# Kernel tuning notes

Hardware: AMD Instinct MI355X
Metric: run time of the kernel (lower is better)

The kernel has to match this reference:

```python
import jax, jax.numpy as jnp
import numpy as np

N = 100000   # nodes
E = 1600000  # edges
D = 64       # in_dim == hidden
H = 64       # hidden
L = 5        # GIN layers
G = 128      # graphs in batch
OUT = 10     # out_dim
BN_EPS = 1e-5


def setup_inputs() -> dict:
    key = jax.random.key(0)
    ks = jax.random.split(key, 16)
    x = jax.random.normal(ks[0], (N, D), dtype=jnp.float32)
    ei = jax.random.randint(ks[1], (2, E), 0, N, dtype=jnp.int64)
    b = jnp.sort(jax.random.randint(ks[2], (N,), 0, G, dtype=jnp.int64))
    s = 0.1
    return {
        "x": x,
        "ei": ei,
        "b": b,
        "conv_W1": jax.random.normal(ks[3], (L, D, H), dtype=jnp.float32) * s,
        "conv_b1": jnp.zeros((L, H), dtype=jnp.float32),
        "conv_W2": jax.random.normal(ks[4], (L, H, H), dtype=jnp.float32) * s,
        "conv_b2": jnp.zeros((L, H), dtype=jnp.float32),
        "bn_gamma": jnp.ones((L, H), dtype=jnp.float32),
        "bn_beta": jnp.zeros((L, H), dtype=jnp.float32),
        "head_W1": jax.random.normal(ks[5], (H, H), dtype=jnp.float32) * s,
        "head_b1": jnp.zeros((H,), dtype=jnp.float32),
        "head_W2": jax.random.normal(ks[6], (H, OUT), dtype=jnp.float32) * s,
        "head_b2": jnp.zeros((OUT,), dtype=jnp.float32),
    }


def reference(x, ei, b, conv_W1, conv_b1, conv_W2, conv_b2,
              bn_gamma, bn_beta, head_W1, head_b1, head_W2, head_b2):
    src, dst = ei[0], ei[1]
    for l in range(L):
        # GINConv (eps=0): h = x + sum_{j in N(i)} x_j  via gather + scatter-add
        agg = jax.ops.segment_sum(x[src], dst, num_segments=N)  # [N, d]
        h = x + agg
        # nn MLP: Linear -> ReLU -> Linear
        h = jax.nn.relu(h @ conv_W1[l] + conv_b1[l]) @ conv_W2[l] + conv_b2[l]
        # BatchNorm over node dim (batch statistics), then ReLU (dropout: eval)
        mean = jnp.mean(h, axis=0)
        var = jnp.var(h, axis=0)
        h = bn_gamma[l] * (h - mean) * jax.lax.rsqrt(var + BN_EPS) + bn_beta[l]
        x = jax.nn.relu(h)
    # global mean pool per graph
    sums = jax.ops.segment_sum(x, b, num_segments=G)                 # [G, H]
    cnts = jax.ops.segment_sum(jnp.ones((N,), x.dtype), b, num_segments=G)
    pooled = sums / jnp.maximum(cnts, 1.0)[:, None]
    # head: Linear -> ReLU -> (Dropout eval) -> Linear
    return jax.nn.relu(pooled @ head_W1 + head_b1) @ head_W2 + head_b2
```

## Files before the change

kernel.cpp:

```cpp
#include <hip/hip_runtime.h>

#define N_NODES 100000
#define N_EDGES 1600000
#define HDIM    64
#define NLAYERS 5
#define NGRAPH  128
#define NOUT    10
#define BN_EPS  1e-5f
#define NBUCK   196
#define EPB     8192
#define NTILES  (N_NODES / 16)

typedef __attribute__((ext_vector_type(8))) short bf16x8;
typedef __attribute__((ext_vector_type(4))) float f32x4;

static __device__ __forceinline__ unsigned short f2bf(float f) {
    unsigned u = __float_as_uint(f);
    unsigned r = (u + 0x7FFFu + ((u >> 16) & 1u)) >> 16;
    return (unsigned short)r;
}
static __device__ __forceinline__ float bf2f(unsigned short h) {
    return __uint_as_float(((unsigned)h) << 16);
}


__global__ __launch_bounds__(256) void k_hist(const int* __restrict__ dst, int* __restrict__ counts) {
    int e = blockIdx.x * 256 + threadIdx.x;
    if (e < N_EDGES) atomicAdd(&counts[dst[e]], 1);
}

__global__ __launch_bounds__(256) void k_scan_bt(const int* __restrict__ counts, int* __restrict__ bsums) {
    __shared__ int sm[256];
    int t = threadIdx.x;
    int base = blockIdx.x * 1024 + t * 4;
    int s = 0;
#pragma unroll
    for (int k = 0; k < 4; ++k) { int i = base + k; s += (i < N_NODES) ? counts[i] : 0; }
    sm[t] = s; __syncthreads();
    for (int o = 128; o > 0; o >>= 1) { if (t < o) sm[t] += sm[t + o]; __syncthreads(); }
    if (t == 0) bsums[blockIdx.x] = sm[0];
}

__global__ void k_scan_tot(int* bsums, int nblk, int* offsets) {
    if (threadIdx.x == 0 && blockIdx.x == 0) {
        int run = 0;
        for (int i = 0; i < nblk; ++i) { int v = bsums[i]; bsums[i] = run; run += v; }
        offsets[N_NODES] = N_EDGES;
    }
}

__global__ __launch_bounds__(256) void k_scan_fin(const int* __restrict__ counts, const int* __restrict__ bsums,
                                                 int* __restrict__ offsets, int* __restrict__ cursor) {
    __shared__ int sm[256];
    int t = threadIdx.x;
    int base = blockIdx.x * 1024 + t * 4;
    int v[4]; int s = 0;
#pragma unroll
    for (int k = 0; k < 4; ++k) { int i = base + k; v[k] = (i < N_NODES) ? counts[i] : 0; s += v[k]; }
    sm[t] = s; __syncthreads();
    for (int o = 1; o < 256; o <<= 1) {
        int add = (t >= o) ? sm[t - o] : 0;
        __syncthreads();
        sm[t] += add;
        __syncthreads();
    }
    int run = bsums[blockIdx.x] + (sm[t] - s);
#pragma unroll
    for (int k = 0; k < 4; ++k) {
        int i = base + k;
        if (i < N_NODES) { offsets[i] = run; cursor[i] = run; run += v[k]; }
    }
}

__global__ void k_binit(const int* __restrict__ offs, int* __restrict__ bcursor) {
    int b = blockIdx.x * 256 + threadIdx.x;
    if (b < NBUCK) bcursor[b] = offs[b << 9];
}

__global__ __launch_bounds__(1024) void k_binfill(const int* __restrict__ src, const int* __restrict__ dst,
                                                  int* __restrict__ bcursor, unsigned* __restrict__ tmp) {
    __shared__ unsigned slots[EPB];
    __shared__ int cnt[NBUCK], lcur[NBUCK], gbase[NBUCK];
    __shared__ int lbase[NBUCK + 1];
    __shared__ int sscan[256];
    int t = threadIdx.x;
    int e0 = blockIdx.x * EPB;
    for (int i = t; i < NBUCK; i += 1024) { cnt[i] = 0; lcur[i] = 0; }
    __syncthreads();
    unsigned pk[8]; int bk[8];
#pragma unroll
    for (int k = 0; k < 8; ++k) {
        int e = e0 + k * 1024 + t;
        bk[k] = -1;
        if (e < N_EDGES) {
            int s = src[e], d = dst[e];
            int b = d >> 9;
            pk[k] = ((unsigned)(d & 511) << 17) | (unsigned)s;
            bk[k] = b;
            atomicAdd(&cnt[b], 1);
        }
    }
    __syncthreads();
    if (t < 256) sscan[t] = (t < NBUCK) ? cnt[t] : 0;
    __syncthreads();
    for (int o = 1; o < 256; o <<= 1) {
        int v = 0;
        if (t < 256 && t >= o) v = sscan[t - o];
        __syncthreads();
        if (t < 256) sscan[t] += v;
        __syncthreads();
    }
    if (t < NBUCK) {
        lbase[t] = sscan[t] - cnt[t];
        gbase[t] = atomicAdd(&bcursor[t], cnt[t]);
    }
    if (t == 0) lbase[NBUCK] = sscan[255];
    __syncthreads();
#pragma unroll
    for (int k = 0; k < 8; ++k) {
        if (bk[k] >= 0) {
            int pos = lbase[bk[k]] + atomicAdd(&lcur[bk[k]], 1);
            slots[pos] = pk[k];
        }
    }
    __syncthreads();
    int total = lbase[NBUCK];
    for (int i = t; i < total; i += 1024) {
        int lo = 0, hi = NBUCK - 1;
        while (lo < hi) { int mid = (lo + hi + 1) >> 1; if (lbase[mid] <= i) lo = mid; else hi = mid - 1; }
        tmp[gbase[lo] + (i - lbase[lo])] = slots[i];
    }
}

__global__ __launch_bounds__(1024) void k_localcsr(const unsigned* __restrict__ tmp, const int* __restrict__ offs,
                                                   int* __restrict__ cursor, int* __restrict__ csr) {
    int b = blockIdx.x;
    int nlo = b << 9;
    int nhi = nlo + 512; if (nhi > N_NODES) nhi = N_NODES;
    int base = offs[nlo], end = offs[nhi];
    for (int i = base + (int)threadIdx.x; i < end; i += 1024) {
        unsigned pk = tmp[i];
        int node = nlo + (int)(pk >> 17);
        int p = atomicAdd(&cursor[node], 1);
        csr[p] = (int)(pk & 0x1FFFFu);
    }
}

__global__ __launch_bounds__(256) void k_wcvt(const float* __restrict__ cW1, const float* __restrict__ cW2,
                                              unsigned short* __restrict__ whi, unsigned short* __restrict__ wlo) {
    int tid = blockIdx.x * 256 + threadIdx.x;
    if (tid >= 5120) return;
    int lane = tid & 63;
    int r = tid >> 6;
    int nt = r & 3;
    int ks = (r >> 2) & 1;
    int gemm = (r >> 3) & 1;
    int layer = r >> 4;
    const float* W = (gemm ? cW2 : cW1) + (size_t)layer * 4096;
    size_t ob = ((size_t)r * 64 + lane) * 8;
#pragma unroll
    for (int j = 0; j < 8; ++j) {
        float w = W[(32 * ks + 8 * (lane >> 4) + j) * 64 + 16 * nt + (lane & 15)];
        unsigned short h = f2bf(w);
        whi[ob + j] = h;
        wlo[ob + j] = f2bf(w - bf2f(h));
    }
}


static __device__ __forceinline__ void bn_coeffs(const float* stats, const float* gam, const float* bet,
                                                 int j0, float4& sc, float4& sh) {
    const float invN = 1.0f / (float)N_NODES;
    float m, v, s;
    m = stats[j0+0]*invN; v = stats[64+j0+0]*invN - m*m; s = gam[j0+0]*rsqrtf(v+BN_EPS); sc.x = s; sh.x = bet[j0+0]-m*s;
    m = stats[j0+1]*invN; v = stats[64+j0+1]*invN - m*m; s = gam[j0+1]*rsqrtf(v+BN_EPS); sc.y = s; sh.y = bet[j0+1]-m*s;
    m = stats[j0+2]*invN; v = stats[64+j0+2]*invN - m*m; s = gam[j0+2]*rsqrtf(v+BN_EPS); sc.z = s; sh.z = bet[j0+2]-m*s;
    m = stats[j0+3]*invN; v = stats[64+j0+3]*invN - m*m; s = gam[j0+3]*rsqrtf(v+BN_EPS); sc.w = s; sh.w = bet[j0+3]-m*s;
}

static __device__ __forceinline__ float4 bn_apply(float4 v, const float4& sc, const float4& sh) {
    v.x = fmaxf(fmaf(v.x, sc.x, sh.x), 0.f);
    v.y = fmaxf(fmaf(v.y, sc.y, sh.y), 0.f);
    v.z = fmaxf(fmaf(v.z, sc.z, sh.z), 0.f);
    v.w = fmaxf(fmaf(v.w, sc.w, sh.w), 0.f);
    return v;
}

template <bool APPLY>
__global__ __launch_bounds__(256) void k_agg(const float4* __restrict__ x4, const int* __restrict__ offsets,
                                             const int* __restrict__ csr, float4* __restrict__ agg4,
                                             const float* __restrict__ stats, const float* __restrict__ gam,
                                             const float* __restrict__ bet) {
    int tid = blockIdx.x * 256 + threadIdx.x;
    int n = tid >> 4, q = tid & 15;
    if (n >= N_NODES) return;
    float4 sc, sh;
    if (APPLY) bn_coeffs(stats, gam, bet, q * 4, sc, sh);
    int beg = offsets[n], end = offsets[n + 1];
    float4 a0 = make_float4(0.f, 0.f, 0.f, 0.f);
    float4 a1 = make_float4(0.f, 0.f, 0.f, 0.f);
    int e = beg;
    for (; e + 1 < end; e += 2) {
        int s0 = csr[e], s1 = csr[e + 1];
        float4 v0 = x4[(size_t)s0 * 16 + q];
        float4 v1 = x4[(size_t)s1 * 16 + q];
        if (APPLY) { v0 = bn_apply(v0, sc, sh); v1 = bn_apply(v1, sc, sh); }
        a0.x += v0.x; a0.y += v0.y; a0.z += v0.z; a0.w += v0.w;
        a1.x += v1.x; a1.y += v1.y; a1.z += v1.z; a1.w += v1.w;
    }
    if (e < end) {
        int s0 = csr[e];
        float4 v0 = x4[(size_t)s0 * 16 + q];
        if (APPLY) v0 = bn_apply(v0, sc, sh);
        a0.x += v0.x; a0.y += v0.y; a0.z += v0.z; a0.w += v0.w;
    }
    a0.x += a1.x; a0.y += a1.y; a0.z += a1.z; a0.w += a1.w;
    agg4[(size_t)n * 16 + q] = a0;
}

template <bool APPLY>
__global__ __launch_bounds__(256) void k_mlp3(const float* __restrict__ x, float* __restrict__ aggh2,
                                              const unsigned short* __restrict__ w1hi, const unsigned short* __restrict__ w1lo,
                                              const unsigned short* __restrict__ w2hi, const unsigned short* __restrict__ w2lo,
                                              const float* __restrict__ b1, const float* __restrict__ b2,
                                              const float* __restrict__ statsPrev, const float* __restrict__ gam,
                                              const float* __restrict__ bet, float* __restrict__ statsOut) {
    __shared__ float h1s[4][16 * 68];
    int t = threadIdx.x;
    int lane = t & 63;
    int wv = t >> 6;
    int lr = lane & 15;
    int lg = lane >> 4;
    int nw = gridDim.x * 4;
    float* myh1 = &h1s[wv][0];

    float sc[16], sh[16];
    if (APPLY) {
        const float invN = 1.0f / (float)N_NODES;
#pragma unroll
        for (int ks = 0; ks < 2; ++ks)
#pragma unroll
            for (int j = 0; j < 8; ++j) {
                int f = 32 * ks + 8 * lg + j;
                float m = statsPrev[f] * invN;
                float v = statsPrev[64 + f] * invN - m * m;
                float s = gam[f] * rsqrtf(v + BN_EPS);
                sc[ks * 8 + j] = s; sh[ks * 8 + j] = bet[f] - m * s;
            }
    }
    float bias1[4], bias2[4];
#pragma unroll
    for (int nt = 0; nt < 4; ++nt) { bias1[nt] = b1[16 * nt + lr]; bias2[nt] = b2[16 * nt + lr]; }

    float st_s[4] = {0.f, 0.f, 0.f, 0.f}, st_q[4] = {0.f, 0.f, 0.f, 0.f};

    for (int base = blockIdx.x * 4; base < NTILES; base += nw) {
        int tile = base + wv;
        bool act = tile < NTILES;
        bf16x8 Ah[2], Al[2];
        f32x4 acc[4];
        if (act) {
            int node = tile * 16 + lr;
#pragma unroll
            for (int ks = 0; ks < 2; ++ks) {
                int f0 = 32 * ks + 8 * lg;
                const float* xr = x + (size_t)node * 64 + f0;
                const float* ar = aggh2 + (size_t)node * 64 + f0;
                float4 xv0 = *(const float4*)xr, xv1 = *(const float4*)(xr + 4);
                float4 av0 = *(const float4*)ar, av1 = *(const float4*)(ar + 4);
                float in[8] = {xv0.x, xv0.y, xv0.z, xv0.w, xv1.x, xv1.y, xv1.z, xv1.w};
                float ag[8] = {av0.x, av0.y, av0.z, av0.w, av1.x, av1.y, av1.z, av1.w};
#pragma unroll
                for (int j = 0; j < 8; ++j) {
                    float v = in[j];
                    if (APPLY) v = fmaxf(fmaf(v, sc[ks * 8 + j], sh[ks * 8 + j]), 0.f);
                    v += ag[j];
                    unsigned short h = f2bf(v);
                    Ah[ks][j] = (short)h;
                    Al[ks][j] = (short)f2bf(v - bf2f(h));
                }
            }
#pragma unroll
            for (int nt = 0; nt < 4; ++nt) {
                f32x4 c = {bias1[nt], bias1[nt], bias1[nt], bias1[nt]};
#pragma unroll
                for (int ks = 0; ks < 2; ++ks) {
                    bf16x8 bh = *(const bf16x8*)(w1hi + ((size_t)((ks * 4 + nt) * 64 + lane)) * 8);
                    bf16x8 bl = *(const bf16x8*)(w1lo + ((size_t)((ks * 4 + nt) * 64 + lane)) * 8);
                    c = __builtin_amdgcn_mfma_f32_16x16x32_bf16(Ah[ks], bh, c, 0, 0, 0);
                    c = __builtin_amdgcn_mfma_f32_16x16x32_bf16(Ah[ks], bl, c, 0, 0, 0);
                    c = __builtin_amdgcn_mfma_f32_16x16x32_bf16(Al[ks], bh, c, 0, 0, 0);
                }
                acc[nt] = c;
            }
#pragma unroll
            for (int nt = 0; nt < 4; ++nt)
#pragma unroll
                for (int r = 0; r < 4; ++r)
                    myh1[(4 * lg + r) * 68 + 16 * nt + lr] = fmaxf(acc[nt][r], 0.f);
        }
        __syncthreads();
        if (act) {
            bf16x8 A2h[2], A2l[2];
#pragma unroll
            for (int ks = 0; ks < 2; ++ks) {
                const float* hr = &myh1[lr * 68 + 32 * ks + 8 * lg];
                float4 h0 = *(const float4*)hr;
                float4 h1v = *(const float4*)(hr + 4);
                float hv[8] = {h0.x, h0.y, h0.z, h0.w, h1v.x, h1v.y, h1v.z, h1v.w};
#pragma unroll
                for (int j = 0; j < 8; ++j) {
                    unsigned short hh = f2bf(hv[j]);
                    A2h[ks][j] = (short)hh;
                    A2l[ks][j] = (short)f2bf(hv[j] - bf2f(hh));
                }
            }
            int nodeb = (base + wv) * 16;
#pragma unroll
            for (int nt = 0; nt < 4; ++nt) {
                f32x4 c = {bias2[nt], bias2[nt], bias2[nt], bias2[nt]};
#pragma unroll
                for (int ks = 0; ks < 2; ++ks) {
                    bf16x8 bh = *(const bf16x8*)(w2hi + ((size_t)((ks * 4 + nt) * 64 + lane)) * 8);
                    bf16x8 bl = *(const bf16x8*)(w2lo + ((size_t)((ks * 4 + nt) * 64 + lane)) * 8);
                    c = __builtin_amdgcn_mfma_f32_16x16x32_bf16(A2h[ks], bh, c, 0, 0, 0);
                    c = __builtin_amdgcn_mfma_f32_16x16x32_bf16(A2h[ks], bl, c, 0, 0, 0);
                    c = __builtin_amdgcn_mfma_f32_16x16x32_bf16(A2l[ks], bh, c, 0, 0, 0);
                }
#pragma unroll
                for (int r = 0; r < 4; ++r) {
                    float v = c[r];
                    aggh2[(size_t)(nodeb + 4 * lg + r) * 64 + 16 * nt + lr] = v;
                    st_s[nt] += v; st_q[nt] += v * v;
                }
            }
        }
        __syncthreads();
    }
#pragma unroll
    for (int nt = 0; nt < 4; ++nt) {
        float s = st_s[nt], q = st_q[nt];
        s += __shfl_xor(s, 16); q += __shfl_xor(q, 16);
        s += __shfl_xor(s, 32); q += __shfl_xor(q, 32);
        if (lg == 0) {
            atomicAdd(&statsOut[16 * nt + lr], s);
            atomicAdd(&statsOut[64 + 16 * nt + lr], q);
        }
    }
}


__global__ void k_bounds(const int* __restrict__ b, int* __restrict__ bounds) {
    int g = threadIdx.x;
    if (g > NGRAPH) return;
    int lo = 0, hi = N_NODES;
    while (lo < hi) { int mid = (lo + hi) >> 1; if (b[mid] < g) lo = mid + 1; else hi = mid; }
    bounds[g] = lo;
}

__global__ __launch_bounds__(256) void k_pool(const float4* __restrict__ x4, const int* __restrict__ bounds,
                                              float4* __restrict__ pooled4, const float* __restrict__ stats,
                                              const float* __restrict__ gam, const float* __restrict__ bet) {
    int g = blockIdx.x;
    int beg = bounds[g], end = bounds[g + 1];
    int t = threadIdx.x;
    int q = t & 15;
    int w = t >> 4;
    float4 sc, sh;
    bn_coeffs(stats, gam, bet, q * 4, sc, sh);
    float4 a = make_float4(0.f, 0.f, 0.f, 0.f);
    for (int n = beg + w; n < end; n += 16) {
        float4 v = bn_apply(x4[(size_t)n * 16 + q], sc, sh);
        a.x += v.x; a.y += v.y; a.z += v.z; a.w += v.w;
    }
    __shared__ float4 sm[16][16];
    sm[w][q] = a; __syncthreads();
    for (int o = 8; o > 0; o >>= 1) {
        if (w < o) {
            float4 u = sm[w + o][q];
            sm[w][q].x += u.x; sm[w][q].y += u.y; sm[w][q].z += u.z; sm[w][q].w += u.w;
        }
        __syncthreads();
    }
    if (w == 0) {
        float inv = (end > beg) ? 1.0f / (float)(end - beg) : 0.0f;
        float4 r = sm[0][q];
        r.x *= inv; r.y *= inv; r.z *= inv; r.w *= inv;
        pooled4[g * 16 + q] = r;
    }
}

__global__ __launch_bounds__(128) void k_head(const float* __restrict__ pooled,
                                              const float* __restrict__ W1, const float* __restrict__ b1,
                                              const float* __restrict__ W2, const float* __restrict__ b2,
                                              float* __restrict__ out) {
    __shared__ float w1s[64 * 64];
    __shared__ float w2s[64 * NOUT];
    int t = threadIdx.x;
    for (int i = t; i < 64 * 64; i += 128) w1s[i] = W1[i];
    for (int i = t; i < 64 * NOUT; i += 128) w2s[i] = W2[i];
    __syncthreads();
    int g = t;
    float pr[64];
#pragma unroll
    for (int k = 0; k < 64; ++k) pr[k] = pooled[g * 64 + k];
    float acc[NOUT];
#pragma unroll
    for (int o = 0; o < NOUT; ++o) acc[o] = b2[o];
    for (int j = 0; j < 64; ++j) {
        float h = b1[j];
#pragma unroll
        for (int k = 0; k < 64; ++k) h = fmaf(pr[k], w1s[k * 64 + j], h);
        h = fmaxf(h, 0.f);
#pragma unroll
        for (int o = 0; o < NOUT; ++o) acc[o] = fmaf(h, w2s[j * NOUT + o], acc[o]);
    }
#pragma unroll
    for (int o = 0; o < NOUT; ++o) out[g * NOUT + o] = acc[o];
}


extern "C" void kernel_launch(void* const* d_in, const int* in_sizes, int n_in,
                              void* d_out, int out_size, void* d_ws, size_t ws_size,
                              hipStream_t stream) {
    const float* x0  = (const float*)d_in[0];
    const int*   ei  = (const int*)d_in[1];
    const int*   b   = (const int*)d_in[2];
    const float* cW1 = (const float*)d_in[3];
    const float* cb1 = (const float*)d_in[4];
    const float* cW2 = (const float*)d_in[5];
    const float* cb2 = (const float*)d_in[6];
    const float* gam = (const float*)d_in[7];
    const float* bet = (const float*)d_in[8];
    const float* hW1 = (const float*)d_in[9];
    const float* hb1 = (const float*)d_in[10];
    const float* hW2 = (const float*)d_in[11];
    const float* hb2 = (const float*)d_in[12];
    float* out = (float*)d_out;

    char* ws = (char*)d_ws;
    size_t off = 0;
    auto alloc = [&](size_t bytes) { void* p = ws + off; off += (bytes + 255) & ~(size_t)255; return p; };
    float* bufA   = (float*)alloc((size_t)N_NODES * 64 * sizeof(float));
    float* bufB   = (float*)alloc((size_t)N_NODES * 64 * sizeof(float));
    int*   csr    = (int*)alloc((size_t)N_EDGES * sizeof(int));
    int*   counts = (int*)alloc((size_t)(N_NODES + 1) * sizeof(int));
    int*   offs   = (int*)alloc((size_t)(N_NODES + 1) * sizeof(int));
    int*   cursor = (int*)alloc((size_t)(N_NODES + 1) * sizeof(int));
    int*   bsums  = (int*)alloc(256 * sizeof(int));
    int*   bcursor= (int*)alloc(256 * sizeof(int));
    float* stats  = (float*)alloc(NLAYERS * 128 * sizeof(float));
    float* pooled = (float*)alloc(NGRAPH * 64 * sizeof(float));
    int*   bounds = (int*)alloc((NGRAPH + 1) * sizeof(int));
    unsigned short* whi = (unsigned short*)alloc(5 * 2 * 4096 * sizeof(unsigned short));
    unsigned short* wlo = (unsigned short*)alloc(5 * 2 * 4096 * sizeof(unsigned short));
    unsigned* tmp = (unsigned*)bufB;

    const int* src = ei;
    const int* dst = ei + N_EDGES;

    hipMemsetAsync(counts, 0, (N_NODES + 1) * sizeof(int), stream);
    hipMemsetAsync(stats, 0, NLAYERS * 128 * sizeof(float), stream);

    const int EB = (N_EDGES + 255) / 256;
    const int SB = (N_NODES + 1023) / 1024;
    const int FB = (N_EDGES + EPB - 1) / EPB;
    k_hist<<<EB, 256, 0, stream>>>(dst, counts);
    k_scan_bt<<<SB, 256, 0, stream>>>(counts, bsums);
    k_scan_tot<<<1, 1, 0, stream>>>(bsums, SB, offs);
    k_scan_fin<<<SB, 256, 0, stream>>>(counts, bsums, offs, cursor);
    k_binit<<<1, 256, 0, stream>>>(offs, bcursor);
    k_binfill<<<FB, 1024, 0, stream>>>(src, dst, bcursor, tmp);
    k_localcsr<<<NBUCK, 1024, 0, stream>>>(tmp, offs, cursor, csr);
    k_bounds<<<1, NGRAPH + 1, 0, stream>>>(b, bounds);
    k_wcvt<<<20, 256, 0, stream>>>(cW1, cW2, whi, wlo);

    const int AB = (N_NODES * 16 + 255) / 256;
    const int MG = 782;

    const float* P = x0;
    float* Q = bufA;
    float* spare = bufB;
    for (int l = 0; l < NLAYERS; ++l) {
        const float* sPrev = stats + (size_t)(l - 1) * 128;
        const float* gPrev = gam + (size_t)(l - 1) * 64;
        const float* bPrev = bet + (size_t)(l - 1) * 64;
        const unsigned short* w1h = whi + (size_t)(l * 2) * 4096;
        const unsigned short* w1l = wlo + (size_t)(l * 2) * 4096;
        const unsigned short* w2h = whi + (size_t)(l * 2 + 1) * 4096;
        const unsigned short* w2l = wlo + (size_t)(l * 2 + 1) * 4096;
        if (l == 0) {
            k_agg<false><<<AB, 256, 0, stream>>>((const float4*)P, offs, csr, (float4*)Q,
                                                 nullptr, nullptr, nullptr);
            k_mlp3<false><<<MG, 256, 0, stream>>>(P, Q, w1h, w1l, w2h, w2l,
                                                  cb1, cb2,
                                                  nullptr, nullptr, nullptr, stats);
        } else {
            k_agg<true><<<AB, 256, 0, stream>>>((const float4*)P, offs, csr, (float4*)Q,
                                                sPrev, gPrev, bPrev);
            k_mlp3<true><<<MG, 256, 0, stream>>>(P, Q, w1h, w1l, w2h, w2l,
                                                 cb1 + l * 64, cb2 + l * 64,
                                                 sPrev, gPrev, bPrev, stats + (size_t)l * 128);
        }
        float* newSpare = (P == x0) ? spare : (float*)P;
        P = Q;
        Q = newSpare;
    }

    k_pool<<<NGRAPH, 256, 0, stream>>>((const float4*)P, bounds, (float4*)pooled,
                                       stats + 4 * 128, gam + 4 * 64, bet + 4 * 64);
    k_head<<<1, 128, 0, stream>>>(pooled, hW1, hb1, hW2, hb2, out);
}
```

Measured before the change: 964.0 us.

## Fold self term into aggregation and prefetch two tiles per wave in MLP

The aggregation kernel now starts its accumulator from the node's own (BN-applied) features, so the MLP kernel no longer re-reads x or recomputes BN coefficients. The MLP kernel drops its grid-stride loop and block-wide __syncthreads, giving each wave exactly two tiles whose inputs are loaded up front to overlap memory latency. The aim is less global traffic and fewer barriers. In exchange the fixed MLP_WAVES constant ties the grid to the node count, and the shared-memory h1 tile is now read back within a wave without an explicit barrier.

```diff
diff --git a/kernel.cpp b/kernel.cpp
--- a/kernel.cpp
+++ b/kernel.cpp
@@ -10,6 +10,7 @@
 #define NBUCK   196
 #define EPB     8192
 #define NTILES  (N_NODES / 16)
+#define MLP_WAVES 3128
 
 typedef __attribute__((ext_vector_type(8))) short bf16x8;
 typedef __attribute__((ext_vector_type(4))) float f32x4;
@@ -197,7 +198,8 @@
     float4 sc, sh;
     if (APPLY) bn_coeffs(stats, gam, bet, q * 4, sc, sh);
     int beg = offsets[n], end = offsets[n + 1];
-    float4 a0 = make_float4(0.f, 0.f, 0.f, 0.f);
+    float4 a0 = x4[(size_t)n * 16 + q];
+    if (APPLY) a0 = bn_apply(a0, sc, sh);
     float4 a1 = make_float4(0.f, 0.f, 0.f, 0.f);
     int e = beg;
     for (; e + 1 < end; e += 2) {
@@ -218,125 +220,105 @@
     agg4[(size_t)n * 16 + q] = a0;
 }
 
-template <bool APPLY>
-__global__ __launch_bounds__(256) void k_mlp3(const float* __restrict__ x, float* __restrict__ aggh2,
+__global__ __launch_bounds__(256) void k_mlp4(float* __restrict__ aggh2,
                                               const unsigned short* __restrict__ w1hi, const unsigned short* __restrict__ w1lo,
                                               const unsigned short* __restrict__ w2hi, const unsigned short* __restrict__ w2lo,
                                               const float* __restrict__ b1, const float* __restrict__ b2,
-                                              const float* __restrict__ statsPrev, const float* __restrict__ gam,
-                                              const float* __restrict__ bet, float* __restrict__ statsOut) {
+                                              float* __restrict__ statsOut) {
     __shared__ float h1s[4][16 * 68];
     int t = threadIdx.x;
     int lane = t & 63;
     int wv = t >> 6;
     int lr = lane & 15;
     int lg = lane >> 4;
-    int nw = gridDim.x * 4;
     float* myh1 = &h1s[wv][0];
 
-    float sc[16], sh[16];
-    if (APPLY) {
-        const float invN = 1.0f / (float)N_NODES;
-#pragma unroll
-        for (int ks = 0; ks < 2; ++ks)
+    float bias1[4], bias2[4];
+#pragma unroll
+    for (int nt = 0; nt < 4; ++nt) { bias1[nt] = b1[16 * nt + lr]; bias2[nt] = b2[16 * nt + lr]; }
+
+    float st_s[4] = {0.f, 0.f, 0.f, 0.f}, st_q[4] = {0.f, 0.f, 0.f, 0.f};
+
+    int tile0 = blockIdx.x * 4 + wv;
+    int tile1 = tile0 + MLP_WAVES;
+    bool act1 = tile1 < NTILES;
+
+    const float4* base0 = (const float4*)(aggh2 + (size_t)(tile0 * 16 + lr) * 64);
+    float4 L0[4], L1[4];
+    L0[0] = base0[2 * lg];     L0[1] = base0[2 * lg + 1];
+    L0[2] = base0[8 + 2 * lg]; L0[3] = base0[8 + 2 * lg + 1];
+    if (act1) {
+        const float4* base1 = (const float4*)(aggh2 + (size_t)(tile1 * 16 + lr) * 64);
+        L1[0] = base1[2 * lg];     L1[1] = base1[2 * lg + 1];
+        L1[2] = base1[8 + 2 * lg]; L1[3] = base1[8 + 2 * lg + 1];
+    }
+
+    auto process = [&](int tile, const float4* L) {
+        bf16x8 Ah[2], Al[2];
+#pragma unroll
+        for (int ks = 0; ks < 2; ++ks) {
+            float in[8] = {L[2*ks].x, L[2*ks].y, L[2*ks].z, L[2*ks].w,
+                           L[2*ks+1].x, L[2*ks+1].y, L[2*ks+1].z, L[2*ks+1].w};
 #pragma unroll
             for (int j = 0; j < 8; ++j) {
-                int f = 32 * ks + 8 * lg + j;
-                float m = statsPrev[f] * invN;
-                float v = statsPrev[64 + f] * invN - m * m;
-                float s = gam[f] * rsqrtf(v + BN_EPS);
-                sc[ks * 8 + j] = s; sh[ks * 8 + j] = bet[f] - m * s;
+                unsigned short h = f2bf(in[j]);
+                Ah[ks][j] = (short)h;
+                Al[ks][j] = (short)f2bf(in[j] - bf2f(h));
             }
-    }
-    float bias1[4], bias2[4];
-#pragma unroll
-    for (int nt = 0; nt < 4; ++nt) { bias1[nt] = b1[16 * nt + lr]; bias2[nt] = b2[16 * nt + lr]; }
-
-    float st_s[4] = {0.f, 0.f, 0.f, 0.f}, st_q[4] = {0.f, 0.f, 0.f, 0.f};
-
-    for (int base = blockIdx.x * 4; base < NTILES; base += nw) {
-        int tile = base + wv;
-        bool act = tile < NTILES;
-        bf16x8 Ah[2], Al[2];
-        f32x4 acc[4];
-        if (act) {
-            int node = tile * 16 + lr;
+        }
+#pragma unroll
+        for (int nt = 0; nt < 4; ++nt) {
+            f32x4 c = {bias1[nt], bias1[nt], bias1[nt], bias1[nt]};
 #pragma unroll
             for (int ks = 0; ks < 2; ++ks) {
-                int f0 = 32 * ks + 8 * lg;
-                const float* xr = x + (size_t)node * 64 + f0;
-                const float* ar = aggh2 + (size_t)node * 64 + f0;
-                float4 xv0 = *(const float4*)xr, xv1 = *(const float4*)(xr + 4);
-                float4 av0 = *(const float4*)ar, av1 = *(const float4*)(ar + 4);
-                float in[8] = {xv0.x, xv0.y, xv0.z, xv0.w, xv1.x, xv1.y, xv1.z, xv1.w};
-                float ag[8] = {av0.x, av0.y, av0.z, av0.w, av1.x, av1.y, av1.z, av1.w};
-#pragma unroll
-                for (int j = 0; j < 8; ++j) {
-                    float v = in[j];
-                    if (APPLY) v = fmaxf(fmaf(v, sc[ks * 8 + j], sh[ks * 8 + j]), 0.f);
-                    v += ag[j];
-                    unsigned short h = f2bf(v);
-                    Ah[ks][j] = (short)h;
-                    Al[ks][j] = (short)f2bf(v - bf2f(h));
-                }
+                bf16x8 bh = *(const bf16x8*)(w1hi + ((size_t)((ks * 4 + nt) * 64 + lane)) * 8);
+                bf16x8 bl = *(const bf16x8*)(w1lo + ((size_t)((ks * 4 + nt) * 64 + lane)) * 8);
+                c = __builtin_amdgcn_mfma_f32_16x16x32_bf16(Ah[ks], bh, c, 0, 0, 0);
+                c = __builtin_amdgcn_mfma_f32_16x16x32_bf16(Ah[ks], bl, c, 0, 0, 0);
+                c = __builtin_amdgcn_mfma_f32_16x16x32_bf16(Al[ks], bh, c, 0, 0, 0);
             }
 #pragma unroll
-            for (int nt = 0; nt < 4; ++nt) {
-                f32x4 c = {bias1[nt], bias1[nt], bias1[nt], bias1[nt]};
-#pragma unroll
-                for (int ks = 0; ks < 2; ++ks) {
-                    bf16x8 bh = *(const bf16x8*)(w1hi + ((size_t)((ks * 4 + nt) * 64 + lane)) * 8);
-                    bf16x8 bl = *(const bf16x8*)(w1lo + ((size_t)((ks * 4 + nt) * 64 + lane)) * 8);
-                    c = __builtin_amdgcn_mfma_f32_16x16x32_bf16(Ah[ks], bh, c, 0, 0, 0);
-                    c = __builtin_amdgcn_mfma_f32_16x16x32_bf16(Ah[ks], bl, c, 0, 0, 0);
-                    c = __builtin_amdgcn_mfma_f32_16x16x32_bf16(Al[ks], bh, c, 0, 0, 0);
-                }
-                acc[nt] = c;
+            for (int r = 0; r < 4; ++r)
+                myh1[(4 * lg + r) * 68 + 16 * nt + lr] = fmaxf(c[r], 0.f);
+        }
+        bf16x8 A2h[2], A2l[2];
+#pragma unroll
+        for (int ks = 0; ks < 2; ++ks) {
+            const float* hr = &myh1[lr * 68 + 32 * ks + 8 * lg];
+            float4 h0 = *(const float4*)hr;
+            float4 h1v = *(const float4*)(hr + 4);
+            float hv[8] = {h0.x, h0.y, h0.z, h0.w, h1v.x, h1v.y, h1v.z, h1v.w};
+#pragma unroll
+            for (int j = 0; j < 8; ++j) {
+                unsigned short hh = f2bf(hv[j]);
+                A2h[ks][j] = (short)hh;
+                A2l[ks][j] = (short)f2bf(hv[j] - bf2f(hh));
             }
-#pragma unroll
-            for (int nt = 0; nt < 4; ++nt)
-#pragma unroll
-                for (int r = 0; r < 4; ++r)
-                    myh1[(4 * lg + r) * 68 + 16 * nt + lr] = fmaxf(acc[nt][r], 0.f);
-        }
-        __syncthreads();
-        if (act) {
-            bf16x8 A2h[2], A2l[2];
+        }
+        int nodeb = tile * 16;
+#pragma unroll
+        for (int nt = 0; nt < 4; ++nt) {
+            f32x4 c = {bias2[nt], bias2[nt], bias2[nt], bias2[nt]};
 #pragma unroll
             for (int ks = 0; ks < 2; ++ks) {
-                const float* hr = &myh1[lr * 68 + 32 * ks + 8 * lg];
-                float4 h0 = *(const float4*)hr;
-                float4 h1v = *(const float4*)(hr + 4);
-                float hv[8] = {h0.x, h0.y, h0.z, h0.w, h1v.x, h1v.y, h1v.z, h1v.w};
-#pragma unroll
-                for (int j = 0; j < 8; ++j) {
-                    unsigned short hh = f2bf(hv[j]);
-                    A2h[ks][j] = (short)hh;
-                    A2l[ks][j] = (short)f2bf(hv[j] - bf2f(hh));
-                }
+                bf16x8 bh = *(const bf16x8*)(w2hi + ((size_t)((ks * 4 + nt) * 64 + lane)) * 8);
+                bf16x8 bl = *(const bf16x8*)(w2lo + ((size_t)((ks * 4 + nt) * 64 + lane)) * 8);
+                c = __builtin_amdgcn_mfma_f32_16x16x32_bf16(A2h[ks], bh, c, 0, 0, 0);
+                c = __builtin_amdgcn_mfma_f32_16x16x32_bf16(A2h[ks], bl, c, 0, 0, 0);
+                c = __builtin_amdgcn_mfma_f32_16x16x32_bf16(A2l[ks], bh, c, 0, 0, 0);
             }
-            int nodeb = (base + wv) * 16;
-#pragma unroll
-            for (int nt = 0; nt < 4; ++nt) {
-                f32x4 c = {bias2[nt], bias2[nt], bias2[nt], bias2[nt]};
-#pragma unroll
-                for (int ks = 0; ks < 2; ++ks) {
-                    bf16x8 bh = *(const bf16x8*)(w2hi + ((size_t)((ks * 4 + nt) * 64 + lane)) * 8);
-                    bf16x8 bl = *(const bf16x8*)(w2lo + ((size_t)((ks * 4 + nt) * 64 + lane)) * 8);
-                    c = __builtin_amdgcn_mfma_f32_16x16x32_bf16(A2h[ks], bh, c, 0, 0, 0);
-                    c = __builtin_amdgcn_mfma_f32_16x16x32_bf16(A2h[ks], bl, c, 0, 0, 0);
-                    c = __builtin_amdgcn_mfma_f32_16x16x32_bf16(A2l[ks], bh, c, 0, 0, 0);
-                }
-#pragma unroll
-                for (int r = 0; r < 4; ++r) {
-                    float v = c[r];
-                    aggh2[(size_t)(nodeb + 4 * lg + r) * 64 + 16 * nt + lr] = v;
-                    st_s[nt] += v; st_q[nt] += v * v;
-                }
+#pragma unroll
+            for (int r = 0; r < 4; ++r) {
+                float v = c[r];
+                aggh2[(size_t)(nodeb + 4 * lg + r) * 64 + 16 * nt + lr] = v;
+                st_s[nt] += v; st_q[nt] += v * v;
             }
         }
-        __syncthreads();
-    }
+    };
+
+    process(tile0, L0);
+    if (act1) process(tile1, L1);
+
 #pragma unroll
     for (int nt = 0; nt < 4; ++nt) {
         float s = st_s[nt], q = st_q[nt];
@@ -476,7 +458,7 @@
     k_wcvt<<<20, 256, 0, stream>>>(cW1, cW2, whi, wlo);
 
     const int AB = (N_NODES * 16 + 255) / 256;
-    const int MG = 782;
+    const int MG = MLP_WAVES / 4;
 
     const float* P = x0;
     float* Q = bufA;
@@ -492,16 +474,13 @@
         if (l == 0) {
             k_agg<false><<<AB, 256, 0, stream>>>((const float4*)P, offs, csr, (float4*)Q,
                                                  nullptr, nullptr, nullptr);
-            k_mlp3<false><<<MG, 256, 0, stream>>>(P, Q, w1h, w1l, w2h, w2l,
-                                                  cb1, cb2,
-                                                  nullptr, nullptr, nullptr, stats);
         } else {
             k_agg<true><<<AB, 256, 0, stream>>>((const float4*)P, offs, csr, (float4*)Q,
                                                 sPrev, gPrev, bPrev);
-            k_mlp3<true><<<MG, 256, 0, stream>>>(P, Q, w1h, w1l, w2h, w2l,
-                                                 cb1 + l * 64, cb2 + l * 64,
-                                                 sPrev, gPrev, bPrev, stats + (size_t)l * 128);
-        }
+        }
+        k_mlp4<<<MG, 256, 0, stream>>>(Q, w1h, w1l, w2h, w2l,
+                                       cb1 + l * 64, cb2 + l * 64,
+                                       stats + (size_t)l * 128);
         float* newSpare = (P == x0) ? spare : (float*)P;
         P = Q;
         Q = newSpare;
```

New measurement: 966.5 us. No clear change (+0.3%).
